# Performance work log

Measured on AMD Instinct MI355X. Metric: run time of the kernel, lower is better.

Reference implementation:

```python
import jax, jax.numpy as jnp
import numpy as np

B, L, D_IN, D_H = 8, 16384, 256, 256  # leaves L = 2**14, complete binary tree
N = 2 * L - 1  # total nodes, heap layout: children of j are 2j+1, 2j+2


def setup_inputs() -> dict:
    key = jax.random.key(0)
    ks = jax.random.split(key, 7)
    s_in = 1.0 / float(np.sqrt(D_IN))
    s_h = 1.0 / float(np.sqrt(D_H))
    return {
        "x": jax.random.normal(ks[0], (B, N, D_IN), jnp.float32),
        "W_iou": jax.random.uniform(ks[1], (D_IN, 3 * D_H), jnp.float32, -s_in, s_in),
        "b_iou": jax.random.uniform(ks[2], (3 * D_H,), jnp.float32, -s_in, s_in),
        "U_iou": jax.random.uniform(ks[3], (D_H, 3 * D_H), jnp.float32, -s_h, s_h),
        "W_f": jax.random.uniform(ks[4], (D_IN, D_H), jnp.float32, -s_in, s_in),
        "b_f": jax.random.uniform(ks[5], (D_IN,)[:0] + (D_H,), jnp.float32, -s_in, s_in),
        "U_f": jax.random.uniform(ks[6], (D_H, D_H), jnp.float32, -s_h, s_h),
    }


def reference(x, W_iou, b_iou, U_iou, W_f, b_f, U_f):
    Bn, Nn, _ = x.shape
    H = U_f.shape[0]
    Lv = (Nn + 1) // 2  # number of leaves
    depth = int(np.log2(Lv))

    # --- leaf nodes (no children): heap indices Lv-1 .. 2Lv-2 ---
    x_leaf = x[:, Lv - 1:, :]                       # [B, L, d_in]
    iou = x_leaf @ W_iou + b_iou                    # [B, L, 3H]
    i, o, u = jnp.split(iou, 3, axis=-1)
    c = jax.nn.sigmoid(i) * jnp.tanh(u)
    h = jax.nn.sigmoid(o) * jnp.tanh(c)             # [B, L, H]

    # --- internal levels, bottom-up; each node has exactly 2 children ---
    n = Lv
    for _ in range(depth):
        n //= 2
        x_lvl = x[:, n - 1:2 * n - 1, :]            # [B, n, d_in]
        hc = h.reshape(Bn, n, 2, H)                 # children hidden states
        cc = c.reshape(Bn, n, 2, H)                 # children cell states
        h_sum = hc.sum(axis=2)                      # child-sum  [B, n, H]
        iou = x_lvl @ W_iou + b_iou + h_sum @ U_iou
        i, o, u = jnp.split(iou, 3, axis=-1)
        # per-child forget gate: sigmoid(W_f x + b_f + U_f h_j)
        f = jax.nn.sigmoid((x_lvl @ W_f + b_f)[:, :, None, :]
                           + jnp.einsum('bnch,hk->bnck', hc, U_f))
        c = jax.nn.sigmoid(i) * jnp.tanh(u) + (f * cc).sum(axis=2)
        h = jax.nn.sigmoid(o) * jnp.tanh(c)

    # root h, c concatenated -> [B, 2H]
    return jnp.concatenate([h[:, 0, :], c[:, 0, :]], axis=-1)
```

## Files before the change

kernel.cpp:

```cpp
#include <hip/hip_runtime.h>
#include <math.h>


#define Bb 8
#define Lleaf 16384
#define Nn 32767
#define Dd 256

typedef __attribute__((ext_vector_type(8))) short short8;
typedef __attribute__((ext_vector_type(4))) float float4v;

__device__ __forceinline__ float sigf(float x) {
    return __builtin_amdgcn_rcpf(1.0f + __expf(-x));
}
__device__ __forceinline__ float tanh_fast(float x) {
    return fmaf(2.0f, sigf(2.0f * x), -1.0f);
}
__device__ __forceinline__ unsigned short f2bf(float f) {
    unsigned int u = __float_as_uint(f);
    u = (u + 0x7FFFu + ((u >> 16) & 1u)) >> 16;
    return (unsigned short)u;
}
__device__ __forceinline__ float bf2f(unsigned short h) {
    return __uint_as_float(((unsigned int)h) << 16);
}
__device__ __forceinline__ void load_lds16(const void* g, void* l) {
    __builtin_amdgcn_global_load_lds(
        (const __attribute__((address_space(1))) unsigned int*)g,
        (__attribute__((address_space(3))) unsigned int*)l, 16, 0, 0);
}

__global__ __launch_bounds__(256) void xcast(
    const float* __restrict__ x, unsigned short* __restrict__ xbf)
{
    const int base = (blockIdx.x * 256 + threadIdx.x) * 8;
    const float4* p = (const float4*)(x + base);
    const float4 f0 = p[0], f1 = p[1];
    union { unsigned short us[8]; uint4 v; } pk;
    pk.us[0] = f2bf(f0.x); pk.us[1] = f2bf(f0.y);
    pk.us[2] = f2bf(f0.z); pk.us[3] = f2bf(f0.w);
    pk.us[4] = f2bf(f1.x); pk.us[5] = f2bf(f1.y);
    pk.us[6] = f2bf(f1.z); pk.us[7] = f2bf(f1.w);
    *(uint4*)(xbf + base) = pk.v;
}

__global__ __launch_bounds__(256) void pack_internal(
    const float* __restrict__ W_iou, const float* __restrict__ U_iou,
    const float* __restrict__ W_f,   const float* __restrict__ U_f,
    unsigned short* __restrict__ Bt)
{
    const int idx = blockIdx.x * 256 + threadIdx.x;
    const int col = idx / 768, k = idx - col * 768;
    const int q = col / 80, rem = col - q * 80;
    const int g = rem >> 4, r = rem & 15;
    const int d = (q << 4) + r;
    const int seg = k >> 8, kk = k & 255;
    float val;
    if (g < 3) {
        val = (seg == 0) ? W_iou[kk * 768 + g * 256 + d]
                         : U_iou[kk * 768 + g * 256 + d];
    } else if (seg == 0) {
        val = W_f[kk * 256 + d];
    } else if (seg == 1) {
        val = (g == 3) ? U_f[kk * 256 + d] : 0.0f;
    } else {
        val = (g == 4) ? U_f[kk * 256 + d] : 0.0f;
    }
    Bt[idx] = f2bf(val);
}

__global__ __launch_bounds__(256) void pack_leaf(
    const float* __restrict__ W_iou, unsigned short* __restrict__ Btl)
{
    const int idx = blockIdx.x * 256 + threadIdx.x;
    const int col = idx >> 8, k = idx & 255;
    const int q = col / 48, rem = col - q * 48;
    const int g = rem >> 4, r = rem & 15;
    const int d = (q << 4) + r;
    Btl[idx] = f2bf(W_iou[k * 768 + g * 256 + d]);
}

__global__ __launch_bounds__(256, 3) void gemm_level_big(
    const unsigned short* __restrict__ xbf, const unsigned short* __restrict__ Bt,
    const float* __restrict__ b_iou, const float* __restrict__ b_f,
    unsigned short* __restrict__ h_out, float* __restrict__ c_out,
    const unsigned short* __restrict__ h_ch, const float* __restrict__ c_ch,
    int n, int lvl)
{
    __shared__ unsigned short Alds[2][128 * 64];
    __shared__ unsigned short Blds[2][80 * 64];
    const int tid  = threadIdx.x;
    const int wave = tid >> 6, lane = tid & 63;
    const int l16  = lane & 15, q4 = lane >> 4;

    const int p     = blockIdx.x;
    const int xcd   = p & 7;
    const int local = p >> 3;
    const int by    = local & 15;
    const int bxl   = local >> 4;
    const int gpx   = n >> 7;
    const int bx    = xcd * gpx + bxl;

    const int m0   = bx * 128;
    const int n0   = by * 80;
    const int lr   = lane >> 3;
    const int lp   = (lane & 7) ^ lr;

    const int b   = m0 >> lvl;
    const int xr0 = m0 + (n - 1) + b * (Nn - n);

    auto stageA = [&](int kk, unsigned short* dst) {
        #pragma unroll
        for (int it = 0; it < 4; ++it) {
            const int g = it * 4 + wave;
            const int r = g * 8 + lr;
            const unsigned short* src;
            if (kk < 4) {
                src = xbf + (((xr0 + r) << 8) + kk * 64 + lp * 8);
            } else {
                const int sel = (kk >= 8) ? 1 : 0;
                src = h_ch + (((2 * (m0 + r) + sel) << 8) + ((kk - 4) & 3) * 64 + lp * 8);
            }
            load_lds16(src, dst + g * 512);
        }
    };
    auto stageB = [&](int kk, unsigned short* dst) {
        #pragma unroll
        for (int it = 0; it < 3; ++it) {
            const int g = it * 4 + wave;
            if (g < 10) {
                const int row = g * 8 + lr;
                load_lds16(Bt + ((n0 + row) * 768 + kk * 64 + lp * 8), dst + g * 512);
            }
        }
    };

    unsigned short* Ac = Alds[0]; unsigned short* An = Alds[1];
    unsigned short* Bc = Blds[0]; unsigned short* Bn = Blds[1];

    stageA(0, Ac); stageB(0, Bc);

    float4v acc[2][5];
    {
        const int d = (by << 4) + l16;
        const float bv[5] = {b_iou[d], b_iou[256 + d], b_iou[512 + d],
                             b_f[d], b_f[d]};
        #pragma unroll
        for (int g = 0; g < 5; ++g) {
            float4v v; v[0] = bv[g]; v[1] = bv[g]; v[2] = bv[g]; v[3] = bv[g];
            acc[0][g] = v; acc[1][g] = v;
        }
    }

    asm volatile("s_waitcnt vmcnt(0)" ::: "memory");
    __builtin_amdgcn_s_barrier();

    for (int kk = 0; kk < 12; ++kk) {
        if (kk < 11) { stageA(kk + 1, An); stageB(kk + 1, Bn); }
        #pragma unroll
        for (int ks = 0; ks < 2; ++ks) {
            const int pa = ks * 4 + q4;
            const int sw = (pa ^ (l16 & 7)) * 8;
            const short8 a0 = *(const short8*)&Ac[(wave * 32 + l16) * 64 + sw];
            const short8 a1 = *(const short8*)&Ac[(wave * 32 + 16 + l16) * 64 + sw];
            #pragma unroll
            for (int ni = 0; ni < 5; ++ni) {
                const short8 bf = *(const short8*)&Bc[(ni * 16 + l16) * 64 + sw];
                acc[0][ni] = __builtin_amdgcn_mfma_f32_16x16x32_bf16(a0, bf, acc[0][ni], 0, 0, 0);
                acc[1][ni] = __builtin_amdgcn_mfma_f32_16x16x32_bf16(a1, bf, acc[1][ni], 0, 0, 0);
            }
        }
        if (kk < 11) {
            asm volatile("s_waitcnt vmcnt(0)" ::: "memory");
            __builtin_amdgcn_s_barrier();
            unsigned short* t = Ac; Ac = An; An = t;
            t = Bc; Bc = Bn; Bn = t;
        }
    }

    #pragma unroll
    for (int mi = 0; mi < 2; ++mi) {
        #pragma unroll
        for (int reg = 0; reg < 4; ++reg) {
            const int row_l = wave * 32 + mi * 16 + (q4 << 2) + reg;
            const int m = m0 + row_l;
            const int cbase = (2 * m) << 8;
            const int obase = m << 8;
            const int d = (by << 4) + l16;
            const float i_ = acc[mi][0][reg];
            const float o_ = acc[mi][1][reg];
            const float u_ = acc[mi][2][reg];
            const float f1 = acc[mi][3][reg];
            const float f2 = acc[mi][4][reg];
            const float c1 = c_ch[cbase + d];
            const float c2 = c_ch[cbase + 256 + d];
            const float c = sigf(i_) * tanh_fast(u_) + sigf(f1) * c1 + sigf(f2) * c2;
            const float h = sigf(o_) * tanh_fast(c);
            c_out[obase + d] = c;
            h_out[obase + d] = f2bf(h);
        }
    }
}

__global__ __launch_bounds__(256, 2) void gemm_level(
    const unsigned short* __restrict__ xbf, const unsigned short* __restrict__ Bt,
    const float* __restrict__ b_iou, const float* __restrict__ b_f,
    unsigned short* __restrict__ h_out, float* __restrict__ c_out,
    const unsigned short* __restrict__ h_ch, const float* __restrict__ c_ch,
    int n, int lvl)
{
    __shared__ unsigned short Alds[2][128 * 64];
    __shared__ unsigned short Blds[2][160 * 64];
    const int tid  = threadIdx.x;
    const int wave = tid >> 6, lane = tid & 63;
    const int l16  = lane & 15, q4 = lane >> 4;
    const int m0   = blockIdx.x * 128;
    const int n0   = blockIdx.y * 160;
    const int lr   = lane >> 3;
    const int lp   = (lane & 7) ^ lr;

    auto stageA = [&](int kk, unsigned short* dst) {
        #pragma unroll
        for (int it = 0; it < 4; ++it) {
            const int g = it * 4 + wave;
            const int r = g * 8 + lr;
            const int m = m0 + r;
            const unsigned short* src;
            if (kk < 4) {
                const int bb = m >> lvl;
                src = xbf + (((m + (n - 1) + bb * (Nn - n)) << 8) + kk * 64 + lp * 8);
            } else {
                const int sel = (kk >= 8) ? 1 : 0;
                src = h_ch + (((2 * m + sel) << 8) + ((kk - 4) & 3) * 64 + lp * 8);
            }
            load_lds16(src, dst + g * 512);
        }
    };
    auto stageB = [&](int kk, unsigned short* dst) {
        #pragma unroll
        for (int it = 0; it < 5; ++it) {
            const int g = it * 4 + wave;
            const int row = g * 8 + lr;
            load_lds16(Bt + ((n0 + row) * 768 + kk * 64 + lp * 8), dst + g * 512);
        }
    };

    unsigned short* Ac = Alds[0]; unsigned short* An = Alds[1];
    unsigned short* Bc = Blds[0]; unsigned short* Bn = Blds[1];

    stageA(0, Ac); stageB(0, Bc);

    float4v acc[2][10];
    #pragma unroll
    for (int qq = 0; qq < 2; ++qq) {
        const int d = ((blockIdx.y * 2 + qq) << 4) + l16;
        float bv0 = b_iou[d], bv1 = b_iou[256 + d], bv2 = b_iou[512 + d];
        float bv3 = b_f[d];
        float bv[5] = {bv0, bv1, bv2, bv3, bv3};
        #pragma unroll
        for (int g = 0; g < 5; ++g) {
            float4v v; v[0] = bv[g]; v[1] = bv[g]; v[2] = bv[g]; v[3] = bv[g];
            acc[0][qq * 5 + g] = v; acc[1][qq * 5 + g] = v;
        }
    }

    asm volatile("s_waitcnt vmcnt(0)" ::: "memory");
    __builtin_amdgcn_s_barrier();

    for (int kk = 0; kk < 12; ++kk) {
        if (kk < 11) { stageA(kk + 1, An); stageB(kk + 1, Bn); }
        #pragma unroll
        for (int ks = 0; ks < 2; ++ks) {
            const int pa = ks * 4 + q4;
            const int sw = (pa ^ (l16 & 7)) * 8;
            const short8 a0 = *(const short8*)&Ac[(wave * 32 + l16) * 64 + sw];
            const short8 a1 = *(const short8*)&Ac[(wave * 32 + 16 + l16) * 64 + sw];
            #pragma unroll
            for (int ni = 0; ni < 10; ++ni) {
                const short8 bf = *(const short8*)&Bc[(ni * 16 + l16) * 64 + sw];
                acc[0][ni] = __builtin_amdgcn_mfma_f32_16x16x32_bf16(a0, bf, acc[0][ni], 0, 0, 0);
                acc[1][ni] = __builtin_amdgcn_mfma_f32_16x16x32_bf16(a1, bf, acc[1][ni], 0, 0, 0);
            }
        }
        if (kk < 11) {
            asm volatile("s_waitcnt vmcnt(0)" ::: "memory");
            __builtin_amdgcn_s_barrier();
            unsigned short* t = Ac; Ac = An; An = t;
            t = Bc; Bc = Bn; Bn = t;
        }
    }

    #pragma unroll
    for (int mi = 0; mi < 2; ++mi) {
        #pragma unroll
        for (int reg = 0; reg < 4; ++reg) {
            const int row_l = wave * 32 + mi * 16 + (q4 << 2) + reg;
            const int m = m0 + row_l;
            const int cbase = (2 * m) << 8;
            const int obase = m << 8;
            #pragma unroll
            for (int qq = 0; qq < 2; ++qq) {
                const int d = ((blockIdx.y * 2 + qq) << 4) + l16;
                const float i_ = acc[mi][qq * 5 + 0][reg];
                const float o_ = acc[mi][qq * 5 + 1][reg];
                const float u_ = acc[mi][qq * 5 + 2][reg];
                const float f1 = acc[mi][qq * 5 + 3][reg];
                const float f2 = acc[mi][qq * 5 + 4][reg];
                const float c1 = c_ch[cbase + d];
                const float c2 = c_ch[cbase + 256 + d];
                const float c = sigf(i_) * tanh_fast(u_) + sigf(f1) * c1 + sigf(f2) * c2;
                const float h = sigf(o_) * tanh_fast(c);
                c_out[obase + d] = c;
                h_out[obase + d] = f2bf(h);
            }
        }
    }
}

__global__ __launch_bounds__(256, 2) void gemm_small(
    const unsigned short* __restrict__ xbf, const unsigned short* __restrict__ Bt,
    const float* __restrict__ b_iou, const float* __restrict__ b_f,
    unsigned short* __restrict__ h_out, float* __restrict__ c_out,
    const unsigned short* __restrict__ h_ch, const float* __restrict__ c_ch,
    int n, int lvl)
{
    __shared__ unsigned short Alds[2][64 * 64];
    __shared__ unsigned short Blds[2][160 * 64];
    const int tid  = threadIdx.x;
    const int wave = tid >> 6, lane = tid & 63;
    const int l16  = lane & 15, q4 = lane >> 4;
    const int n0   = blockIdx.y * 160;
    const int lr   = lane >> 3;
    const int lp   = (lane & 7) ^ lr;
    const int rmax = 8 * n - 1;

    auto stageA = [&](int kk, unsigned short* dst) {
        #pragma unroll
        for (int it = 0; it < 2; ++it) {
            const int g = it * 4 + wave;
            const int r = g * 8 + lr;
            const int m = (r > rmax) ? rmax : r;
            const unsigned short* src;
            if (kk < 4) {
                const int bb = m >> lvl;
                src = xbf + (((m + (n - 1) + bb * (Nn - n)) << 8) + kk * 64 + lp * 8);
            } else {
                const int sel = (kk >= 8) ? 1 : 0;
                src = h_ch + (((2 * m + sel) << 8) + ((kk - 4) & 3) * 64 + lp * 8);
            }
            load_lds16(src, dst + g * 512);
        }
    };
    auto stageB = [&](int kk, unsigned short* dst) {
        #pragma unroll
        for (int it = 0; it < 5; ++it) {
            const int g = it * 4 + wave;
            const int row = g * 8 + lr;
            load_lds16(Bt + ((n0 + row) * 768 + kk * 64 + lp * 8), dst + g * 512);
        }
    };

    unsigned short* Ac = Alds[0]; unsigned short* An = Alds[1];
    unsigned short* Bc = Blds[0]; unsigned short* Bn = Blds[1];

    stageA(0, Ac); stageB(0, Bc);

    float4v acc[10];
    #pragma unroll
    for (int qq = 0; qq < 2; ++qq) {
        const int d = ((blockIdx.y * 2 + qq) << 4) + l16;
        float bv0 = b_iou[d], bv1 = b_iou[256 + d], bv2 = b_iou[512 + d];
        float bv3 = b_f[d];
        float bv[5] = {bv0, bv1, bv2, bv3, bv3};
        #pragma unroll
        for (int g = 0; g < 5; ++g) {
            float4v v; v[0] = bv[g]; v[1] = bv[g]; v[2] = bv[g]; v[3] = bv[g];
            acc[qq * 5 + g] = v;
        }
    }

    asm volatile("s_waitcnt vmcnt(0)" ::: "memory");
    __builtin_amdgcn_s_barrier();

    for (int kk = 0; kk < 12; ++kk) {
        if (kk < 11) { stageA(kk + 1, An); stageB(kk + 1, Bn); }
        #pragma unroll
        for (int ks = 0; ks < 2; ++ks) {
            const int pa = ks * 4 + q4;
            const int sw = (pa ^ (l16 & 7)) * 8;
            const short8 a0 = *(const short8*)&Ac[(wave * 16 + l16) * 64 + sw];
            #pragma unroll
            for (int ni = 0; ni < 10; ++ni) {
                const short8 bf = *(const short8*)&Bc[(ni * 16 + l16) * 64 + sw];
                acc[ni] = __builtin_amdgcn_mfma_f32_16x16x32_bf16(a0, bf, acc[ni], 0, 0, 0);
            }
        }
        if (kk < 11) {
            asm volatile("s_waitcnt vmcnt(0)" ::: "memory");
            __builtin_amdgcn_s_barrier();
            unsigned short* t = Ac; Ac = An; An = t;
            t = Bc; Bc = Bn; Bn = t;
        }
    }

    #pragma unroll
    for (int reg = 0; reg < 4; ++reg) {
        const int row_l = wave * 16 + (q4 << 2) + reg;
        const int m = (row_l > rmax) ? rmax : row_l;
        const bool valid = (row_l <= rmax);
        const int cbase = (2 * m) << 8;
        const int obase = m << 8;
        #pragma unroll
        for (int qq = 0; qq < 2; ++qq) {
            const int d = ((blockIdx.y * 2 + qq) << 4) + l16;
            const float i_ = acc[qq * 5 + 0][reg];
            const float o_ = acc[qq * 5 + 1][reg];
            const float u_ = acc[qq * 5 + 2][reg];
            const float f1 = acc[qq * 5 + 3][reg];
            const float f2 = acc[qq * 5 + 4][reg];
            const float c1 = c_ch[cbase + d];
            const float c2 = c_ch[cbase + 256 + d];
            const float c = sigf(i_) * tanh_fast(u_) + sigf(f1) * c1 + sigf(f2) * c2;
            const float h = sigf(o_) * tanh_fast(c);
            if (valid) {
                c_out[obase + d] = c;
                h_out[obase + d] = f2bf(h);
            }
        }
    }
}

__global__ __launch_bounds__(256, 2) void gemm_leaf(
    const unsigned short* __restrict__ xbf, const unsigned short* __restrict__ Btl,
    const float* __restrict__ b_iou,
    unsigned short* __restrict__ h_out, float* __restrict__ c_out)
{
    __shared__ unsigned short Alds[2][128 * 64];
    __shared__ unsigned short Blds[2][96 * 64];
    const int tid  = threadIdx.x;
    const int wave = tid >> 6, lane = tid & 63;
    const int l16  = lane & 15, q4 = lane >> 4;

    const int p     = blockIdx.x;
    const int xcd   = p & 7;
    const int local = p >> 3;
    const int by    = local & 7;
    const int bx    = xcd * 128 + (local >> 3);

    const int m0   = bx * 128;
    const int n0   = by * 96;
    const int lr   = lane >> 3;
    const int lp   = (lane & 7) ^ lr;

    const int b   = m0 >> 14;
    const int xr0 = m0 + (Lleaf - 1) + b * (Nn - Lleaf);

    auto stageA = [&](int kk, unsigned short* dst) {
        #pragma unroll
        for (int it = 0; it < 4; ++it) {
            const int g = it * 4 + wave;
            const int r = g * 8 + lr;
            load_lds16(xbf + (((xr0 + r) << 8) + kk * 64 + lp * 8), dst + g * 512);
        }
    };
    auto stageB = [&](int kk, unsigned short* dst) {
        #pragma unroll
        for (int it = 0; it < 3; ++it) {
            const int g = it * 4 + wave;
            const int row = g * 8 + lr;
            load_lds16(Btl + ((n0 + row) * 256 + kk * 64 + lp * 8), dst + g * 512);
        }
    };

    unsigned short* Ac = Alds[0]; unsigned short* An = Alds[1];
    unsigned short* Bc = Blds[0]; unsigned short* Bn = Blds[1];

    stageA(0, Ac); stageB(0, Bc);

    float4v acc[2][6];
    #pragma unroll
    for (int qq = 0; qq < 2; ++qq) {
        const int d = ((by * 2 + qq) << 4) + l16;
        float bv[3] = {b_iou[d], b_iou[256 + d], b_iou[512 + d]};
        #pragma unroll
        for (int g = 0; g < 3; ++g) {
            float4v v; v[0] = bv[g]; v[1] = bv[g]; v[2] = bv[g]; v[3] = bv[g];
            acc[0][qq * 3 + g] = v; acc[1][qq * 3 + g] = v;
        }
    }

    asm volatile("s_waitcnt vmcnt(0)" ::: "memory");
    __builtin_amdgcn_s_barrier();

    for (int kk = 0; kk < 4; ++kk) {
        if (kk < 3) { stageA(kk + 1, An); stageB(kk + 1, Bn); }
        #pragma unroll
        for (int ks = 0; ks < 2; ++ks) {
            const int pa = ks * 4 + q4;
            const int sw = (pa ^ (l16 & 7)) * 8;
            const short8 a0 = *(const short8*)&Ac[(wave * 32 + l16) * 64 + sw];
            const short8 a1 = *(const short8*)&Ac[(wave * 32 + 16 + l16) * 64 + sw];
            #pragma unroll
            for (int ni = 0; ni < 6; ++ni) {
                const short8 bf = *(const short8*)&Bc[(ni * 16 + l16) * 64 + sw];
                acc[0][ni] = __builtin_amdgcn_mfma_f32_16x16x32_bf16(a0, bf, acc[0][ni], 0, 0, 0);
                acc[1][ni] = __builtin_amdgcn_mfma_f32_16x16x32_bf16(a1, bf, acc[1][ni], 0, 0, 0);
            }
        }
        if (kk < 3) {
            asm volatile("s_waitcnt vmcnt(0)" ::: "memory");
            __builtin_amdgcn_s_barrier();
            unsigned short* t = Ac; Ac = An; An = t;
            t = Bc; Bc = Bn; Bn = t;
        }
    }

    #pragma unroll
    for (int mi = 0; mi < 2; ++mi) {
        #pragma unroll
        for (int reg = 0; reg < 4; ++reg) {
            const int row_l = wave * 32 + mi * 16 + (q4 << 2) + reg;
            const int obase = (m0 + row_l) << 8;
            #pragma unroll
            for (int qq = 0; qq < 2; ++qq) {
                const int d = ((by * 2 + qq) << 4) + l16;
                const float i_ = acc[mi][qq * 3 + 0][reg];
                const float o_ = acc[mi][qq * 3 + 1][reg];
                const float u_ = acc[mi][qq * 3 + 2][reg];
                const float c = sigf(i_) * tanh_fast(u_);
                const float h = sigf(o_) * tanh_fast(c);
                c_out[obase + d] = c;
                h_out[obase + d] = f2bf(h);
            }
        }
    }
}

__global__ __launch_bounds__(256) void out_kernel(
    const unsigned short* __restrict__ h_root, const float* __restrict__ c_root,
    float* __restrict__ out)
{
    const int t = threadIdx.x;
    const int b = blockIdx.x;
    out[b * 512 + t]       = bf2f(h_root[(b << 8) + t]);
    out[b * 512 + 256 + t] = c_root[(b << 8) + t];
}

extern "C" void kernel_launch(void* const* d_in, const int* in_sizes, int n_in,
                              void* d_out, int out_size, void* d_ws, size_t ws_size,
                              hipStream_t stream) {
    const float* x     = (const float*)d_in[0];
    const float* W_iou = (const float*)d_in[1];
    const float* b_iou = (const float*)d_in[2];
    const float* U_iou = (const float*)d_in[3];
    const float* W_f   = (const float*)d_in[4];
    const float* b_f   = (const float*)d_in[5];
    const float* U_f   = (const float*)d_in[6];
    float* out = (float*)d_out;

    char* p = (char*)d_ws;
    unsigned short* xbf = (unsigned short*)p;  p += (size_t)Bb * Nn * Dd * 2;
    float* cE = (float*)p;                     p += (size_t)Bb * Lleaf * Dd * 4;
    float* cO = (float*)p;                     p += (size_t)Bb * (Lleaf/2) * Dd * 4;
    unsigned short* hE = (unsigned short*)p;   p += (size_t)Bb * Lleaf * Dd * 2;
    unsigned short* hO = (unsigned short*)p;   p += (size_t)Bb * (Lleaf/2) * Dd * 2;
    unsigned short* Bt  = (unsigned short*)p;  p += 1280 * 768 * 2;
    unsigned short* Btl = (unsigned short*)p;

    xcast<<<(Bb * Nn * Dd) / (256 * 8), 256, 0, stream>>>(x, xbf);
    pack_internal<<<(1280 * 768) / 256, 256, 0, stream>>>(W_iou, U_iou, W_f, U_f, Bt);
    pack_leaf<<<(768 * 256) / 256, 256, 0, stream>>>(W_iou, Btl);

    gemm_leaf<<<(Bb * Lleaf / 128) * 8, 256, 0, stream>>>(xbf, Btl, b_iou, hE, cE);

    for (int lvl = 13; lvl >= 7; --lvl) {
        const int n = 1 << lvl;
        unsigned short* ho = (lvl & 1) ? hO : hE;  float* co = (lvl & 1) ? cO : cE;
        unsigned short* hc = (lvl & 1) ? hE : hO;  float* cc = (lvl & 1) ? cE : cO;
        gemm_level_big<<<(Bb * n / 128) * 16, 256, 0, stream>>>(
            xbf, Bt, b_iou, b_f, ho, co, hc, cc, n, lvl);
    }
    for (int lvl = 6; lvl >= 4; --lvl) {
        const int n = 1 << lvl;
        unsigned short* ho = (lvl & 1) ? hO : hE;  float* co = (lvl & 1) ? cO : cE;
        unsigned short* hc = (lvl & 1) ? hE : hO;  float* cc = (lvl & 1) ? cE : cO;
        gemm_level<<<dim3(Bb * n / 128, 8), 256, 0, stream>>>(
            xbf, Bt, b_iou, b_f, ho, co, hc, cc, n, lvl);
    }
    for (int lvl = 3; lvl >= 0; --lvl) {
        const int n = 1 << lvl;
        unsigned short* ho = (lvl & 1) ? hO : hE;  float* co = (lvl & 1) ? cO : cE;
        unsigned short* hc = (lvl & 1) ? hE : hO;  float* cc = (lvl & 1) ? cE : cO;
        gemm_small<<<dim3(1, 8), 256, 0, stream>>>(
            xbf, Bt, b_iou, b_f, ho, co, hc, cc, n, lvl);
    }
    out_kernel<<<Bb, 256, 0, stream>>>(hE, cE, out);
}
```

Measured before the change: 1.013 ms.

## Widen level GEMM tile to 128x160 and read B fragments directly from global

The internal-level GEMM kernel now computes a 128x160 output tile per block, arranged as a 2x2 wave grid with 64x80 per wave, and launches half as many blocks. The B (weight) operand is no longer staged through LDS. Each lane loads its MFMA fragments straight from global memory, relying on cache for reuse, which removes the B LDS traffic and its share of the barrier stalls. The risks are higher register pressure from the 4x5 accumulator array at 3 blocks/CU, and global-load latency on B sitting directly in the MFMA loop with no prefetch.

New measurement: 1.349 ms. +33.1%, slower.

```diff
diff --git a/kernel.cpp b/kernel.cpp
--- a/kernel.cpp
+++ b/kernel.cpp
@@ -88,21 +88,20 @@
     int n, int lvl)
 {
     __shared__ unsigned short Alds[2][128 * 64];
-    __shared__ unsigned short Blds[2][80 * 64];
     const int tid  = threadIdx.x;
     const int wave = tid >> 6, lane = tid & 63;
     const int l16  = lane & 15, q4 = lane >> 4;
+    const int wm   = wave >> 1, wn = wave & 1;
 
     const int p     = blockIdx.x;
     const int xcd   = p & 7;
     const int local = p >> 3;
-    const int by    = local & 15;
-    const int bxl   = local >> 4;
-    const int gpx   = n >> 7;
-    const int bx    = xcd * gpx + bxl;
+    const int by    = local & 7;
+    const int bxl   = local >> 3;
+    const int bx    = xcd * (n >> 7) + bxl;
 
     const int m0   = bx * 128;
-    const int n0   = by * 80;
+    const int n0   = by * 160;
     const int lr   = lane >> 3;
     const int lp   = (lane & 7) ^ lr;
 
@@ -124,31 +123,26 @@
             load_lds16(src, dst + g * 512);
         }
     };
-    auto stageB = [&](int kk, unsigned short* dst) {
-        #pragma unroll
-        for (int it = 0; it < 3; ++it) {
-            const int g = it * 4 + wave;
-            if (g < 10) {
-                const int row = g * 8 + lr;
-                load_lds16(Bt + ((n0 + row) * 768 + kk * 64 + lp * 8), dst + g * 512);
-            }
-        }
-    };
+
+    const unsigned short* bp[5];
+    #pragma unroll
+    for (int ni = 0; ni < 5; ++ni)
+        bp[ni] = Bt + (n0 + wn * 80 + ni * 16 + l16) * 768 + (q4 << 3);
 
     unsigned short* Ac = Alds[0]; unsigned short* An = Alds[1];
-    unsigned short* Bc = Blds[0]; unsigned short* Bn = Blds[1];
-
-    stageA(0, Ac); stageB(0, Bc);
-
-    float4v acc[2][5];
+
+    stageA(0, Ac);
+
+    float4v acc[4][5];
     {
-        const int d = (by << 4) + l16;
+        const int d = ((by * 2 + wn) << 4) + l16;
         const float bv[5] = {b_iou[d], b_iou[256 + d], b_iou[512 + d],
                              b_f[d], b_f[d]};
         #pragma unroll
         for (int g = 0; g < 5; ++g) {
             float4v v; v[0] = bv[g]; v[1] = bv[g]; v[2] = bv[g]; v[3] = bv[g];
-            acc[0][g] = v; acc[1][g] = v;
+            #pragma unroll
+            for (int mi = 0; mi < 4; ++mi) acc[mi][g] = v;
         }
     }
 
@@ -156,37 +150,40 @@
     __builtin_amdgcn_s_barrier();
 
     for (int kk = 0; kk < 12; ++kk) {
-        if (kk < 11) { stageA(kk + 1, An); stageB(kk + 1, Bn); }
+        if (kk < 11) stageA(kk + 1, An);
         #pragma unroll
         for (int ks = 0; ks < 2; ++ks) {
             const int pa = ks * 4 + q4;
             const int sw = (pa ^ (l16 & 7)) * 8;
-            const short8 a0 = *(const short8*)&Ac[(wave * 32 + l16) * 64 + sw];
-            const short8 a1 = *(const short8*)&Ac[(wave * 32 + 16 + l16) * 64 + sw];
+            short8 a[4];
+            #pragma unroll
+            for (int mi = 0; mi < 4; ++mi)
+                a[mi] = *(const short8*)&Ac[(wm * 64 + mi * 16 + l16) * 64 + sw];
             #pragma unroll
             for (int ni = 0; ni < 5; ++ni) {
-                const short8 bf = *(const short8*)&Bc[(ni * 16 + l16) * 64 + sw];
-                acc[0][ni] = __builtin_amdgcn_mfma_f32_16x16x32_bf16(a0, bf, acc[0][ni], 0, 0, 0);
-                acc[1][ni] = __builtin_amdgcn_mfma_f32_16x16x32_bf16(a1, bf, acc[1][ni], 0, 0, 0);
+                const short8 bf = *(const short8*)(bp[ni] + kk * 64 + ks * 32);
+                #pragma unroll
+                for (int mi = 0; mi < 4; ++mi)
+                    acc[mi][ni] = __builtin_amdgcn_mfma_f32_16x16x32_bf16(
+                        a[mi], bf, acc[mi][ni], 0, 0, 0);
             }
         }
         if (kk < 11) {
             asm volatile("s_waitcnt vmcnt(0)" ::: "memory");
             __builtin_amdgcn_s_barrier();
             unsigned short* t = Ac; Ac = An; An = t;
-            t = Bc; Bc = Bn; Bn = t;
-        }
-    }
-
-    #pragma unroll
-    for (int mi = 0; mi < 2; ++mi) {
+        }
+    }
+
+    const int d = ((by * 2 + wn) << 4) + l16;
+    #pragma unroll
+    for (int mi = 0; mi < 4; ++mi) {
         #pragma unroll
         for (int reg = 0; reg < 4; ++reg) {
-            const int row_l = wave * 32 + mi * 16 + (q4 << 2) + reg;
+            const int row_l = wm * 64 + mi * 16 + (q4 << 2) + reg;
             const int m = m0 + row_l;
             const int cbase = (2 * m) << 8;
             const int obase = m << 8;
-            const int d = (by << 4) + l16;
             const float i_ = acc[mi][0][reg];
             const float o_ = acc[mi][1][reg];
             const float u_ = acc[mi][2][reg];
@@ -577,7 +574,7 @@
         const int n = 1 << lvl;
         unsigned short* ho = (lvl & 1) ? hO : hE;  float* co = (lvl & 1) ? cO : cE;
         unsigned short* hc = (lvl & 1) ? hE : hO;  float* cc = (lvl & 1) ? cE : cO;
-        gemm_level_big<<<(Bb * n / 128) * 16, 256, 0, stream>>>(
+        gemm_level_big<<<(Bb * n / 128) * 8, 256, 0, stream>>>(
             xbf, Bt, b_iou, b_f, ho, co, hc, cc, n, lvl);
     }
     for (int lvl = 6; lvl >= 4; --lvl) {
```
